# Performance work log

Measured on AMD Instinct MI355X. Metric: run time of the kernel, lower is better.

The kernel has to match this reference:

```python
import jax, jax.numpy as jnp
import numpy as np
import functools, math

HEADS = 16


def _query_chunk_attention(query, key, value, precision, key_chunk_size=4096):
    # query: (q_chunk, bh, d); key/value: (kv, bh, d)
    num_kv, num_heads, k_features = key.shape[-3:]
    v_features = value.shape[-1]
    key_chunk_size = min(key_chunk_size, num_kv)
    query = query / jnp.sqrt(k_features)

    @functools.partial(jax.checkpoint, prevent_cse=False)
    def summarize_chunk(query, key, value):
        attn_weights = jnp.einsum("...qhd,...khd->...qhk", query, key, precision=precision)
        max_score = jnp.max(attn_weights, axis=-1, keepdims=True)
        max_score = jax.lax.stop_gradient(max_score)
        exp_weights = jnp.exp(attn_weights - max_score)
        exp_values = jnp.einsum("...vhf,...qhv->...qhf", value, exp_weights, precision=precision)
        max_score = jnp.einsum("...qhk->...qh", max_score)
        return exp_values, exp_weights.sum(axis=-1), max_score

    def chunk_scanner(chunk_idx):
        key_chunk = jax.lax.dynamic_slice(
            key, [chunk_idx, 0, 0], [key_chunk_size, num_heads, k_features])
        value_chunk = jax.lax.dynamic_slice(
            value, [chunk_idx, 0, 0], [key_chunk_size, num_heads, v_features])
        return summarize_chunk(query, key_chunk, value_chunk)

    chunk_values, chunk_weights, chunk_max = jax.lax.map(
        chunk_scanner, xs=jnp.arange(0, num_kv, key_chunk_size))
    # online softmax rescaling across kv chunks
    global_max = jnp.max(chunk_max, axis=0, keepdims=True)
    max_diffs = jnp.exp(chunk_max - global_max)
    chunk_values = chunk_values * jnp.expand_dims(max_diffs, axis=-1)
    chunk_weights = chunk_weights * max_diffs
    all_values = chunk_values.sum(axis=0)
    all_weights = jnp.expand_dims(chunk_weights, -1).sum(axis=0)
    return all_values / all_weights


def jax_memory_efficient_attention(query, key, value,
                                   precision=jax.lax.Precision.HIGHEST,
                                   query_chunk_size=1024, key_chunk_size=4096):
    # query: (q_len, bh, d)
    num_q, num_heads, q_features = query.shape[-3:]

    def chunk_scanner(chunk_idx, _):
        query_chunk = jax.lax.dynamic_slice(
            query, [chunk_idx, 0, 0],
            [min(query_chunk_size, num_q), num_heads, q_features])
        return (chunk_idx + query_chunk_size,
                _query_chunk_attention(query_chunk, key, value, precision, key_chunk_size))

    _, res = jax.lax.scan(chunk_scanner, 0, xs=None,
                          length=math.ceil(num_q / query_chunk_size))
    return jnp.concatenate(res, axis=-3)


def _reshape_heads_to_batch_dim(tensor, heads):
    b, s, d = tensor.shape
    t = tensor.reshape(b, s, heads, d // heads).transpose(0, 2, 1, 3)
    return t.reshape(b * heads, s, d // heads)


def _attention_fwd(query, key, value):
    heads = HEADS
    q = _reshape_heads_to_batch_dim(query, heads).transpose(1, 0, 2)  # (s, b*h, dh)
    k = _reshape_heads_to_batch_dim(key, heads).transpose(1, 0, 2)
    v = _reshape_heads_to_batch_dim(value, heads).transpose(1, 0, 2)
    flatten_latent_dim = q.shape[-3]
    if flatten_latent_dim % 64 == 0:
        query_chunk_size = flatten_latent_dim // 64
    elif flatten_latent_dim % 16 == 0:
        query_chunk_size = flatten_latent_dim // 16
    elif flatten_latent_dim % 4 == 0:
        query_chunk_size = flatten_latent_dim // 4
    else:
        query_chunk_size = flatten_latent_dim
    out = jax_memory_efficient_attention(q, k, v,
                                         query_chunk_size=query_chunk_size,
                                         key_chunk_size=4096 * 4)
    return out.transpose(1, 0, 2)  # (b*h, s, dh)


def setup_inputs() -> dict:
    key = jax.random.key(0)
    k1, k2, k3 = jax.random.split(key, 3)
    B, S, D = 2, 4096, 1024
    return {
        "query": jax.random.normal(k1, (B, S, D), dtype=jnp.float32),
        "key": jax.random.normal(k2, (B, S, D), dtype=jnp.float32),
        "value": jax.random.normal(k3, (B, S, D), dtype=jnp.float32),
    }


def reference(query, key, value):
    return _attention_fwd(query, key, value)
```

## Files before the change

kernel.cpp:

```cpp
#include <hip/hip_runtime.h>
#include <math.h>

#define SEQ    4096
#define DH     64
#define DMODEL 1024
#define NBH    32
#define KTS    128
#define NTS    (SEQ / KTS)
#define LOG2E  1.44269504088896340736f

typedef __attribute__((ext_vector_type(8)))  short short8;
typedef __attribute__((ext_vector_type(4)))  float f32x4;
typedef __attribute__((ext_vector_type(16))) float f32x16;
typedef __attribute__((ext_vector_type(2)))  unsigned uint2v;

__device__ __forceinline__ unsigned short f2bf(float f) {
  union { float f; unsigned u; } x; x.f = f;
  unsigned r = x.u + 0x7FFFu + ((x.u >> 16) & 1u);
  return (unsigned short)(r >> 16);
}

__device__ __forceinline__ unsigned cvtpk_bf16(float lo, float hi) {
  unsigned r;
  asm("v_cvt_pk_bf16_f32 %0, %1, %2" : "=v"(r) : "v"(lo), "v"(hi));
  return r;
}

__global__ __launch_bounds__(256)
void prep(const float* __restrict__ Kp, const float* __restrict__ Vp,
          unsigned short* __restrict__ ws) {
  __shared__ unsigned short Kt[KTS * DH];
  __shared__ unsigned short Vt[KTS * DH];
  const int blk = blockIdx.x;
  const int bh = blk >> 5, t = blk & 31;
  const int b = bh >> 4, h = bh & 15;
  const size_t gbase = (size_t)b * SEQ * DMODEL + (size_t)h * DH +
                       (size_t)t * KTS * DMODEL;
  const float* Kb = Kp + gbase;
  const float* Vb = Vp + gbase;
  unsigned short* wt = ws + (size_t)blk * 16384;
  const int tid = threadIdx.x;

#pragma unroll
  for (int c = 0; c < 8; ++c) {
    const int idx = c * 256 + tid;
    const int row = idx >> 4, dc = idx & 15;
    f32x4 kf = *(const f32x4*)(Kb + (size_t)row * DMODEL + dc * 4);
    f32x4 vf = *(const f32x4*)(Vb + (size_t)row * DMODEL + dc * 4);
    uint2v ku, vu;
    ku[0] = (unsigned)f2bf(kf[0]) | ((unsigned)f2bf(kf[1]) << 16);
    ku[1] = (unsigned)f2bf(kf[2]) | ((unsigned)f2bf(kf[3]) << 16);
    vu[0] = (unsigned)f2bf(vf[0]) | ((unsigned)f2bf(vf[1]) << 16);
    vu[1] = (unsigned)f2bf(vf[2]) | ((unsigned)f2bf(vf[3]) << 16);
    *(uint2v*)&Kt[row * 64 + dc * 4] = ku;
    *(uint2v*)&Vt[row * 64 + dc * 4] = vu;
  }
  __syncthreads();

#pragma unroll
  for (int c = 0; c < 4; ++c) {
    const int idx = c * 256 + tid;
    const int l31 = idx & 31, hi = (idx >> 5) & 1, d4 = (idx >> 6) & 3, kb = idx >> 8;
    short8 v = *(const short8*)&Kt[(kb * 32 + l31) * 64 + d4 * 16 + hi * 8];
    *(short8*)&wt[idx * 8] = v;
  }
#pragma unroll
  for (int c = 0; c < 4; ++c) {
    const int idx = c * 256 + tid;
    const int l31 = idx & 31, dt = (idx >> 5) & 1, hi = (idx >> 6) & 1, k16 = idx >> 7;
    const int d = dt * 32 + l31, kb0 = k16 * 16 + hi * 8;
    short8 v;
#pragma unroll
    for (int j = 0; j < 8; ++j) v[j] = (short)Vt[(kb0 + j) * 64 + d];
    *(short8*)&wt[8192 + idx * 8] = v;
  }
}

__global__ __launch_bounds__(256, 2)
void fattn(const float* __restrict__ Qp,
           const unsigned short* __restrict__ ws,
           float* __restrict__ Op) {
  __shared__ __align__(16) char lds[2][32768];

  const int tid  = threadIdx.x;
  const int lane = tid & 63;
  const int w    = tid >> 6;
  const int hi   = lane >> 5;
  const int l31  = lane & 31;

  const int id  = blockIdx.x;
  const int rid = (id & 7) * 64 + (id >> 3);
  const int bh  = rid >> 4;
  const int qt  = rid & 15;
  const int q0  = qt * 256 + w * 64;

  const int b = bh >> 4, h = bh & 15;
  const float* Qb = Qp + (size_t)b * SEQ * DMODEL + (size_t)h * DH;
  const char* wsb = (const char*)(ws + (size_t)bh * NTS * 16384);

  short8 qb[2][4];
#pragma unroll
  for (int s = 0; s < 2; ++s) {
    const float* qr = Qb + (size_t)(q0 + s * 32 + l31) * DMODEL;
    const float sc = 0.125f * LOG2E;
#pragma unroll
    for (int d4 = 0; d4 < 4; ++d4) {
      const float* p = qr + d4 * 16 + hi * 8;
      f32x4 f0 = *(const f32x4*)p;
      f32x4 f1 = *(const f32x4*)(p + 4);
      short8 v;
#pragma unroll
      for (int i = 0; i < 4; ++i) {
        v[i]     = (short)f2bf(f0[i] * sc);
        v[i + 4] = (short)f2bf(f1[i] * sc);
      }
      qb[s][d4] = v;
    }
  }

  f32x16 ZERO;
#pragma unroll
  for (int r = 0; r < 16; ++r) ZERO[r] = 0.f;

  f32x16 acc[2][2];
#pragma unroll
  for (int s = 0; s < 2; ++s)
#pragma unroll
    for (int dt = 0; dt < 2; ++dt) acc[s][dt] = ZERO;
  float lsum[2] = {0.f, 0.f};

  const int laneK = hi * 512 + l31 * 16;
  const int laneV = hi * 1024 + l31 * 16;

#define STAGE(buf_, t_)                                                       \
  {                                                                           \
    const char* src_ = wsb + (size_t)(t_) * 32768;                            \
    char* dst_ = &lds[buf_][0];                                               \
    _Pragma("unroll")                                                         \
    for (int c_ = 0; c_ < 8; ++c_) {                                          \
      __builtin_amdgcn_global_load_lds(                                       \
          (const __attribute__((address_space(1))) void*)(src_ + c_ * 4096 +  \
                                                          w * 1024 + lane * 16), \
          (__attribute__((address_space(3))) void*)(dst_ + c_ * 4096 +        \
                                                    w * 1024),                \
          16, 0, 0);                                                          \
    }                                                                         \
  }

  STAGE(0, 0);
  __syncthreads();

  for (int t = 0; t < NTS; ++t) {
    const int buf = t & 1;
    if (t + 1 < NTS) STAGE(buf ^ 1, t + 1);
    const char* Lk = &lds[buf][0];
    const char* Lv = &lds[buf][16384];

#pragma unroll
    for (int kb = 0; kb < 4; ++kb) {
      short8 ka[4];
#pragma unroll
      for (int d4 = 0; d4 < 4; ++d4)
        ka[d4] = *(const short8*)(Lk + kb * 4096 + d4 * 1024 + laneK);
      f32x16 zA, zB;
      __builtin_amdgcn_s_setprio(1);
      zA = __builtin_amdgcn_mfma_f32_32x32x16_bf16(ka[0], qb[0][0], ZERO, 0, 0, 0);
      zB = __builtin_amdgcn_mfma_f32_32x32x16_bf16(ka[0], qb[1][0], ZERO, 0, 0, 0);
      zA = __builtin_amdgcn_mfma_f32_32x32x16_bf16(ka[1], qb[0][1], zA, 0, 0, 0);
      zB = __builtin_amdgcn_mfma_f32_32x32x16_bf16(ka[1], qb[1][1], zB, 0, 0, 0);
      zA = __builtin_amdgcn_mfma_f32_32x32x16_bf16(ka[2], qb[0][2], zA, 0, 0, 0);
      zB = __builtin_amdgcn_mfma_f32_32x32x16_bf16(ka[2], qb[1][2], zB, 0, 0, 0);
      zA = __builtin_amdgcn_mfma_f32_32x32x16_bf16(ka[3], qb[0][3], zA, 0, 0, 0);
      zB = __builtin_amdgcn_mfma_f32_32x32x16_bf16(ka[3], qb[1][3], zB, 0, 0, 0);
      __builtin_amdgcn_s_setprio(0);

#pragma unroll
      for (int r = 0; r < 16; ++r) zA[r] = __builtin_amdgcn_exp2f(zA[r]);
#pragma unroll
      for (int r = 0; r < 16; ++r) zB[r] = __builtin_amdgcn_exp2f(zB[r]);
      {
        float a0 = (zA[0] + zA[1]) + (zA[2] + zA[3]);
        float a1 = (zA[4] + zA[5]) + (zA[6] + zA[7]);
        float a2 = (zA[8] + zA[9]) + (zA[10] + zA[11]);
        float a3 = (zA[12] + zA[13]) + (zA[14] + zA[15]);
        lsum[0] += (a0 + a1) + (a2 + a3);
        float b0 = (zB[0] + zB[1]) + (zB[2] + zB[3]);
        float b1 = (zB[4] + zB[5]) + (zB[6] + zB[7]);
        float b2 = (zB[8] + zB[9]) + (zB[10] + zB[11]);
        float b3 = (zB[12] + zB[13]) + (zB[14] + zB[15]);
        lsum[1] += (b0 + b1) + (b2 + b3);
      }

#pragma unroll
      for (int s = 0; s < 2; ++s) {
        const int R = 8 * s;
        unsigned a0 = cvtpk_bf16(zA[R + 0], zA[R + 1]);
        unsigned c0 = cvtpk_bf16(zA[R + 4], zA[R + 5]);
        unsigned a1 = cvtpk_bf16(zA[R + 2], zA[R + 3]);
        unsigned c1 = cvtpk_bf16(zA[R + 6], zA[R + 7]);
        asm("v_permlane32_swap_b32 %0, %1" : "+v"(a0), "+v"(c0));
        asm("v_permlane32_swap_b32 %0, %1" : "+v"(a1), "+v"(c1));
        union { unsigned u[4]; short8 s8; } pwA;
        pwA.u[0] = a0; pwA.u[1] = a1; pwA.u[2] = c0; pwA.u[3] = c1;
        unsigned d0 = cvtpk_bf16(zB[R + 0], zB[R + 1]);
        unsigned e0 = cvtpk_bf16(zB[R + 4], zB[R + 5]);
        unsigned d1 = cvtpk_bf16(zB[R + 2], zB[R + 3]);
        unsigned e1 = cvtpk_bf16(zB[R + 6], zB[R + 7]);
        asm("v_permlane32_swap_b32 %0, %1" : "+v"(d0), "+v"(e0));
        asm("v_permlane32_swap_b32 %0, %1" : "+v"(d1), "+v"(e1));
        union { unsigned u[4]; short8 s8; } pwB;
        pwB.u[0] = d0; pwB.u[1] = d1; pwB.u[2] = e0; pwB.u[3] = e1;

        const int k16 = kb * 2 + s;
        short8 vb0 = *(const short8*)(Lv + k16 * 2048 + laneV);
        short8 vb1 = *(const short8*)(Lv + k16 * 2048 + 512 + laneV);
        __builtin_amdgcn_s_setprio(1);
        acc[0][0] = __builtin_amdgcn_mfma_f32_32x32x16_bf16(pwA.s8, vb0, acc[0][0], 0, 0, 0);
        acc[0][1] = __builtin_amdgcn_mfma_f32_32x32x16_bf16(pwA.s8, vb1, acc[0][1], 0, 0, 0);
        acc[1][0] = __builtin_amdgcn_mfma_f32_32x32x16_bf16(pwB.s8, vb0, acc[1][0], 0, 0, 0);
        acc[1][1] = __builtin_amdgcn_mfma_f32_32x32x16_bf16(pwB.s8, vb1, acc[1][1], 0, 0, 0);
        __builtin_amdgcn_s_setprio(0);
      }
    }
    __syncthreads();
  }

#pragma unroll
  for (int s = 0; s < 2; ++s) {
    const float lt  = lsum[s] + __shfl_xor(lsum[s], 32, 64);
    const float inv = 1.0f / lt;
#pragma unroll
    for (int dt = 0; dt < 2; ++dt)
#pragma unroll
      for (int r = 0; r < 16; ++r) {
        const int qrow = (r & 3) + 8 * (r >> 2) + 4 * hi;
        const float iv = __shfl(inv, qrow + (lane & 32), 64);
        const size_t row = (size_t)bh * SEQ + q0 + s * 32 + qrow;
        Op[row * DH + dt * 32 + l31] = acc[s][dt][r] * iv;
      }
  }
}

extern "C" void kernel_launch(void* const* d_in, const int* in_sizes, int n_in,
                              void* d_out, int out_size, void* d_ws, size_t ws_size,
                              hipStream_t stream) {
  const float* Q = (const float*)d_in[0];
  const float* K = (const float*)d_in[1];
  const float* V = (const float*)d_in[2];
  float* O = (float*)d_out;
  unsigned short* ws = (unsigned short*)d_ws;

  prep<<<dim3(NBH * NTS), dim3(256), 0, stream>>>(K, V, ws);
  fattn<<<dim3(512), dim3(256), 0, stream>>>(Q, ws, O);
}
```

Before: 155.2 us.

## Split KV range across two blocks per query tile and add combine kernel

Shrinks the KV tile from 128 to 64 keys, which halves LDS use per buffer, and re-lays out the workspace to match. When the workspace is large enough, it launches 1024 attention blocks, each covering half the KV sequence. Each block writes unnormalized bf16 partial outputs and row sums, and a new combine kernel adds the two halves and normalizes them. This targets low occupancy (512 blocks on 256 CUs) but adds an extra launch, partial-result traffic, and bf16 rounding of the partial sums. The softmax max is never tracked, so summing the exponentials is consistent with the existing code.

```diff
diff --git a/kernel.cpp b/kernel.cpp
--- a/kernel.cpp
+++ b/kernel.cpp
@@ -5,8 +5,7 @@
 #define DH     64
 #define DMODEL 1024
 #define NBH    32
-#define KTS    128
-#define NTS    (SEQ / KTS)
+#define NT64   64
 #define LOG2E  1.44269504088896340736f
 
 typedef __attribute__((ext_vector_type(8)))  short short8;
@@ -14,12 +13,18 @@
 typedef __attribute__((ext_vector_type(16))) float f32x16;
 typedef __attribute__((ext_vector_type(2)))  unsigned uint2v;
 
+#define WS_KV_BYTES   33554432ull
+#define WS_NEED_SPLIT 68157440ull
+
 __device__ __forceinline__ unsigned short f2bf(float f) {
   union { float f; unsigned u; } x; x.f = f;
   unsigned r = x.u + 0x7FFFu + ((x.u >> 16) & 1u);
   return (unsigned short)(r >> 16);
 }
-
+__device__ __forceinline__ float bf2f(unsigned short u) {
+  union { unsigned u; float f; } x; x.u = ((unsigned)u) << 16;
+  return x.f;
+}
 __device__ __forceinline__ unsigned cvtpk_bf16(float lo, float hi) {
   unsigned r;
   asm("v_cvt_pk_bf16_f32 %0, %1, %2" : "=v"(r) : "v"(lo), "v"(hi));
@@ -29,16 +34,16 @@
 __global__ __launch_bounds__(256)
 void prep(const float* __restrict__ Kp, const float* __restrict__ Vp,
           unsigned short* __restrict__ ws) {
-  __shared__ unsigned short Kt[KTS * DH];
-  __shared__ unsigned short Vt[KTS * DH];
+  __shared__ unsigned short Kt[128 * DH];
+  __shared__ unsigned short Vt[128 * DH];
   const int blk = blockIdx.x;
-  const int bh = blk >> 5, t = blk & 31;
+  const int bh = blk >> 5, t128 = blk & 31;
   const int b = bh >> 4, h = bh & 15;
   const size_t gbase = (size_t)b * SEQ * DMODEL + (size_t)h * DH +
-                       (size_t)t * KTS * DMODEL;
+                       (size_t)t128 * 128 * DMODEL;
   const float* Kb = Kp + gbase;
   const float* Vb = Vp + gbase;
-  unsigned short* wt = ws + (size_t)blk * 16384;
+  unsigned short* wt = ws + (size_t)bh * NT64 * 8192 + (size_t)(2 * t128) * 8192;
   const int tid = threadIdx.x;
 
 #pragma unroll
@@ -61,26 +66,29 @@
   for (int c = 0; c < 4; ++c) {
     const int idx = c * 256 + tid;
     const int l31 = idx & 31, hi = (idx >> 5) & 1, d4 = (idx >> 6) & 3, kb = idx >> 8;
+    const int tau = kb >> 1, kb2 = kb & 1;
     short8 v = *(const short8*)&Kt[(kb * 32 + l31) * 64 + d4 * 16 + hi * 8];
-    *(short8*)&wt[idx * 8] = v;
+    *(short8*)&wt[tau * 8192 + (((kb2 * 4 + d4) * 2 + hi) * 32 + l31) * 8] = v;
   }
 #pragma unroll
   for (int c = 0; c < 4; ++c) {
     const int idx = c * 256 + tid;
     const int l31 = idx & 31, dt = (idx >> 5) & 1, hi = (idx >> 6) & 1, k16 = idx >> 7;
+    const int tau = k16 >> 2, k162 = k16 & 3;
     const int d = dt * 32 + l31, kb0 = k16 * 16 + hi * 8;
     short8 v;
 #pragma unroll
     for (int j = 0; j < 8; ++j) v[j] = (short)Vt[(kb0 + j) * 64 + d];
-    *(short8*)&wt[8192 + idx * 8] = v;
-  }
-}
-
+    *(short8*)&wt[tau * 8192 + 4096 + (((k162 * 2 + hi) * 64) + dt * 32 + l31) * 8] = v;
+  }
+}
+
+template <bool SPLIT>
 __global__ __launch_bounds__(256, 2)
 void fattn(const float* __restrict__ Qp,
            const unsigned short* __restrict__ ws,
            float* __restrict__ Op) {
-  __shared__ __align__(16) char lds[2][32768];
+  __shared__ __align__(16) char lds[2][16384];
 
   const int tid  = threadIdx.x;
   const int lane = tid & 63;
@@ -88,15 +96,23 @@
   const int hi   = lane >> 5;
   const int l31  = lane & 31;
 
-  const int id  = blockIdx.x;
-  const int rid = (id & 7) * 64 + (id >> 3);
-  const int bh  = rid >> 4;
-  const int qt  = rid & 15;
-  const int q0  = qt * 256 + w * 64;
+  int bh, qt, sh, rid;
+  if (SPLIT) {
+    const int id = blockIdx.x;
+    rid = (id & 7) * 128 + (id >> 3);
+    bh = rid >> 5; qt = (rid >> 1) & 15; sh = rid & 1;
+  } else {
+    const int id = blockIdx.x;
+    rid = (id & 7) * 64 + (id >> 3);
+    bh = rid >> 4; qt = rid & 15; sh = 0;
+  }
+  const int NTloc = SPLIT ? 32 : 64;
+  const int t0    = sh * 32;
+  const int q0    = qt * 256 + w * 64;
 
   const int b = bh >> 4, h = bh & 15;
   const float* Qb = Qp + (size_t)b * SEQ * DMODEL + (size_t)h * DH;
-  const char* wsb = (const char*)(ws + (size_t)bh * NTS * 16384);
+  const char* wsb = (const char*)(ws + (size_t)bh * NT64 * 8192);
 
   short8 qb[2][4];
 #pragma unroll
@@ -121,7 +137,6 @@
   f32x16 ZERO;
 #pragma unroll
   for (int r = 0; r < 16; ++r) ZERO[r] = 0.f;
-
   f32x16 acc[2][2];
 #pragma unroll
   for (int s = 0; s < 2; ++s)
@@ -132,32 +147,32 @@
   const int laneK = hi * 512 + l31 * 16;
   const int laneV = hi * 1024 + l31 * 16;
 
-#define STAGE(buf_, t_)                                                       \
+#define STAGE(buf_, tau_)                                                     \
   {                                                                           \
-    const char* src_ = wsb + (size_t)(t_) * 32768;                            \
+    const char* src_ = wsb + (size_t)(tau_) * 16384;                          \
     char* dst_ = &lds[buf_][0];                                               \
     _Pragma("unroll")                                                         \
-    for (int c_ = 0; c_ < 8; ++c_) {                                          \
+    for (int c_ = 0; c_ < 4; ++c_) {                                          \
       __builtin_amdgcn_global_load_lds(                                       \
           (const __attribute__((address_space(1))) void*)(src_ + c_ * 4096 +  \
-                                                          w * 1024 + lane * 16), \
+                                                          tid * 16),          \
           (__attribute__((address_space(3))) void*)(dst_ + c_ * 4096 +        \
-                                                    w * 1024),                \
+                                                    tid * 16),                \
           16, 0, 0);                                                          \
     }                                                                         \
   }
 
-  STAGE(0, 0);
+  STAGE(0, t0);
   __syncthreads();
 
-  for (int t = 0; t < NTS; ++t) {
+  for (int t = 0; t < NTloc; ++t) {
     const int buf = t & 1;
-    if (t + 1 < NTS) STAGE(buf ^ 1, t + 1);
+    if (t + 1 < NTloc) STAGE(buf ^ 1, t0 + t + 1);
     const char* Lk = &lds[buf][0];
-    const char* Lv = &lds[buf][16384];
-
-#pragma unroll
-    for (int kb = 0; kb < 4; ++kb) {
+    const char* Lv = &lds[buf][8192];
+
+#pragma unroll
+    for (int kb = 0; kb < 2; ++kb) {
       short8 ka[4];
 #pragma unroll
       for (int d4 = 0; d4 < 4; ++d4)
@@ -225,20 +240,63 @@
     __syncthreads();
   }
 
-#pragma unroll
-  for (int s = 0; s < 2; ++s) {
-    const float lt  = lsum[s] + __shfl_xor(lsum[s], 32, 64);
-    const float inv = 1.0f / lt;
-#pragma unroll
-    for (int dt = 0; dt < 2; ++dt)
-#pragma unroll
-      for (int r = 0; r < 16; ++r) {
-        const int qrow = (r & 3) + 8 * (r >> 2) + 4 * hi;
-        const float iv = __shfl(inv, qrow + (lane & 32), 64);
-        const size_t row = (size_t)bh * SEQ + q0 + s * 32 + qrow;
-        Op[row * DH + dt * 32 + l31] = acc[s][dt][r] * iv;
-      }
-  }
+  if (SPLIT) {
+    unsigned short* part = (unsigned short*)((char*)nullptr);
+    part = (unsigned short*)((const char*)ws + WS_KV_BYTES) + (size_t)rid * 16384;
+    float* lout = (float*)((const char*)ws + WS_KV_BYTES + WS_KV_BYTES) + (size_t)rid * 256;
+#pragma unroll
+    for (int s = 0; s < 2; ++s) {
+      const float lt = lsum[s] + __shfl_xor(lsum[s], 32, 64);
+      if (hi == 0) lout[w * 64 + s * 32 + l31] = lt;
+#pragma unroll
+      for (int dt = 0; dt < 2; ++dt)
+#pragma unroll
+        for (int r = 0; r < 16; ++r) {
+          const int qrow = (r & 3) + 8 * (r >> 2) + 4 * hi;
+          part[(w * 64 + s * 32 + qrow) * 64 + dt * 32 + l31] = f2bf(acc[s][dt][r]);
+        }
+    }
+  } else {
+#pragma unroll
+    for (int s = 0; s < 2; ++s) {
+      const float lt  = lsum[s] + __shfl_xor(lsum[s], 32, 64);
+      const float inv = 1.0f / lt;
+#pragma unroll
+      for (int dt = 0; dt < 2; ++dt)
+#pragma unroll
+        for (int r = 0; r < 16; ++r) {
+          const int qrow = (r & 3) + 8 * (r >> 2) + 4 * hi;
+          const float iv = __shfl(inv, qrow + (lane & 32), 64);
+          const size_t row = (size_t)bh * SEQ + q0 + s * 32 + qrow;
+          Op[row * DH + dt * 32 + l31] = acc[s][dt][r] * iv;
+        }
+    }
+  }
+}
+
+__global__ __launch_bounds__(256)
+void combine(const unsigned short* __restrict__ ws, float* __restrict__ Op) {
+  const unsigned short* part = (const unsigned short*)((const char*)ws + WS_KV_BYTES);
+  const float* lsum = (const float*)((const char*)ws + 2 * WS_KV_BYTES);
+  const int gid = blockIdx.x * 256 + threadIdx.x;
+  const int bq = gid >> 11;
+  const int rem = gid & 2047;
+  const int q = rem >> 3, dc = rem & 7;
+  const int pid0 = bq * 2, pid1 = pid0 + 1;
+  short8 A0 = *(const short8*)&part[(size_t)pid0 * 16384 + q * 64 + dc * 8];
+  short8 A1 = *(const short8*)&part[(size_t)pid1 * 16384 + q * 64 + dc * 8];
+  const float l = lsum[pid0 * 256 + q] + lsum[pid1 * 256 + q];
+  const float inv = 1.0f / l;
+  const int bh = bq >> 4, qt = bq & 15;
+  float* o = Op + ((size_t)bh * SEQ + qt * 256 + q) * DH + dc * 8;
+  f32x4 o0, o1;
+#pragma unroll
+  for (int j = 0; j < 4; ++j) {
+    o0[j] = (bf2f((unsigned short)A0[j]) + bf2f((unsigned short)A1[j])) * inv;
+    o1[j] = (bf2f((unsigned short)A0[j + 4]) + bf2f((unsigned short)A1[j + 4])) * inv;
+  }
+  *(f32x4*)o = o0;
+  *(f32x4*)(o + 4) = o1;
 }
 
 extern "C" void kernel_launch(void* const* d_in, const int* in_sizes, int n_in,
@@ -250,6 +308,11 @@
   float* O = (float*)d_out;
   unsigned short* ws = (unsigned short*)d_ws;
 
-  prep<<<dim3(NBH * NTS), dim3(256), 0, stream>>>(K, V, ws);
-  fattn<<<dim3(512), dim3(256), 0, stream>>>(Q, ws, O);
-}
+  prep<<<dim3(NBH * 32), dim3(256), 0, stream>>>(K, V, ws);
+  if (ws_size >= WS_NEED_SPLIT) {
+    fattn<true><<<dim3(1024), dim3(256), 0, stream>>>(Q, ws, O);
+    combine<<<dim3(4096), dim3(256), 0, stream>>>(ws, O);
+  } else {
+    fattn<false><<<dim3(512), dim3(256), 0, stream>>>(Q, ws, O);
+  }
+}
```

Result: slower. 165.4 us (+6.6%).
